# Performance work log

Hardware: AMD Instinct MI355X
Metric: run time of the kernel (lower is better)

The kernel has to match this reference:

```python
import jax, jax.numpy as jnp
import numpy as np

GROUP_SIZE = 128


def dequantize_int4(packed, scales, group_size=GROUP_SIZE, dtype=jnp.float16):
    # packed: [O, I//2] bytes; low nibble -> even cols, high nibble -> odd cols
    O = packed.shape[0]
    I = packed.shape[1] * 2
    low = (packed & 15).astype(jnp.int8) - 8
    high = ((packed >> 4) & 15).astype(jnp.int8) - 8
    unpacked = jnp.stack([low, high], axis=-1).reshape(O, I)  # interleave low/high
    G = I // group_size
    grouped = unpacked.reshape(O, G, group_size).astype(jnp.float32)
    deq = grouped * scales.astype(jnp.float32)[:, :, None]  # per-group scale
    return deq.reshape(O, I).astype(dtype)


def setup_inputs() -> dict:
    key = jax.random.key(0)
    k1, k2, k3 = jax.random.split(key, 3)
    B, S, IN, OUT = 4, 2048, 4096, 11008
    G = IN // GROUP_SIZE
    x = jax.random.normal(k1, (B, S, IN), dtype=jnp.float16)
    packed = jax.random.randint(k2, (OUT, IN // 2), 0, 256, dtype=jnp.int32)
    scales = (jax.random.uniform(k3, (OUT, G), dtype=jnp.float32) * 0.05 + 0.001).astype(jnp.float16)
    return {"x": x, "packed": packed, "scales": scales}


def reference(x, packed, scales):
    x = x.astype(jnp.float16)
    W = dequantize_int4(packed, scales)  # [OUT, IN] fp16
    # nn.functional.linear: x @ W^T
    return jnp.einsum('bsi,oi->bso', x, W)
```

## Files before the change

kernel.cpp:

```cpp
#include <hip/hip_runtime.h>

#define M_DIM 8192
#define N_DIM 11008
#define K_DIM 4096
#define GROUPS 32
#define WQROW 512
#define LDSK 72

typedef short s16x8 __attribute__((ext_vector_type(8)));
typedef _Float16 f16x8 __attribute__((ext_vector_type(8)));
typedef _Float16 h2 __attribute__((ext_vector_type(2)));
typedef float f32x4 __attribute__((ext_vector_type(4)));
typedef unsigned short u16;
typedef unsigned int u32;

union f32u { float f; unsigned u; };
union h16u { u16 u; _Float16 h; };

__device__ __forceinline__ u16 f2bf(float f) {
  f32u v; v.f = f;
  unsigned r = v.u + 0x7FFFu + ((v.u >> 16) & 1u);
  return (u16)(r >> 16);
}
__device__ __forceinline__ float bf2f(u16 b) {
  f32u v; v.u = ((unsigned)b) << 16; return v.f;
}
__device__ __forceinline__ float h2f(u16 b) {
  h16u v; v.u = b; return (float)v.h;
}

__global__ void probe_mode_kernel(const void* __restrict__ scales,
                                  int* __restrict__ mode_out) {
  __shared__ int cnt[3];
  int t = threadIdx.x;
  if (t < 3) cnt[t] = 0;
  __syncthreads();
  float f0 = ((const float*)scales)[t];
  u16  hu  = ((const u16*)scales)[t];
  float f1 = h2f(hu);
  float f2 = bf2f(hu);
  if (f0 > 0.0004f && f0 < 0.065f) atomicAdd(&cnt[0], 1);
  if (f1 > 0.0004f && f1 < 0.065f) atomicAdd(&cnt[1], 1);
  if (f2 > 0.0004f && f2 < 0.065f) atomicAdd(&cnt[2], 1);
  __syncthreads();
  if (t == 0) {
    int m;
    if      (cnt[1] >= 240) m = 1;
    else if (cnt[2] >= 240) m = 2;
    else                    m = 0;
    mode_out[0] = m;
  }
}

__global__ __launch_bounds__(256) void convert_x_nat_kernel(
    const float* __restrict__ xf, u16* __restrict__ xh,
    const int* __restrict__ modep) {
  if (modep && modep[0] != 0) return;
  const int total8 = M_DIM * (K_DIM / 8);
  int idx = blockIdx.x * 256 + threadIdx.x;
  const int stride = gridDim.x * 256;
  for (; idx < total8; idx += stride) {
    const float4* p = (const float4*)(xf + (size_t)idx * 8);
    float4 a = p[0], b = p[1];
    union { _Float16 h[8]; s16x8 v; } r;
    r.h[0] = (_Float16)a.x; r.h[1] = (_Float16)a.y;
    r.h[2] = (_Float16)a.z; r.h[3] = (_Float16)a.w;
    r.h[4] = (_Float16)b.x; r.h[5] = (_Float16)b.y;
    r.h[6] = (_Float16)b.z; r.h[7] = (_Float16)b.w;
    *(s16x8*)(xh + (size_t)idx * 8) = r.v;
  }
}

__global__ __launch_bounds__(256) void dequant_w_kernel(
    const int* __restrict__ packed, const float* __restrict__ scf,
    u16* __restrict__ wf, const int* __restrict__ modep) {
  if (modep && modep[0] != 0) return;
  const int total = N_DIM * (K_DIM / 8);
  int idx = blockIdx.x * 256 + threadIdx.x;
  const int stride = gridDim.x * 256;
  for (; idx < total; idx += stride) {
    const int col = idx >> 9;
    const int d   = idx & 511;
    const float s = scf[col * GROUPS + (d >> 4)];
    const int4 p  = ((const int4*)packed)[idx];
    const int vals[4] = {p.x, p.y, p.z, p.w};
    union { _Float16 h[8]; s16x8 v; } r;
    #pragma unroll
    for (int e = 0; e < 4; ++e) {
      int b = vals[e] & 255;
      r.h[2 * e]     = (_Float16)((float)((b & 15) - 8) * s);
      r.h[2 * e + 1] = (_Float16)((float)(((b >> 4) & 15) - 8) * s);
    }
    *(s16x8*)(wf + (size_t)idx * 8) = r.v;
  }
}

__global__ __launch_bounds__(512, 2) void q4gemm_big_kernel(
    const u16* __restrict__ xh,
    const u16* __restrict__ wf,
    float* __restrict__ out,
    const int* __restrict__ modep)
{
  if (modep && modep[0] != 0) return;

  __shared__ _Float16 AsA[2][256 * 64];
  __shared__ _Float16 AsB[2][256 * 64];

  const int tid  = threadIdx.x;
  const int lane = tid & 63;
  const int wv   = tid >> 6;
  const int wm   = (wv >> 2) * 128;
  const int wn   = (wv & 3) * 64;
  const int ln15 = lane & 15;
  const int lk   = lane >> 4;

  int bid = blockIdx.x;
  int f   = (bid & 7) * 172 + (bid >> 3);
  int bn  = f / 32;
  int bm  = f - bn * 32;
  const int m0 = bm * 256;
  const int n0 = bn * 256;

  const int srow  = lane >> 3;
  const int sperm = (lane & 7) ^ srow;
  const u16* abase[4];
  const u16* bbase[4];
  #pragma unroll
  for (int q = 0; q < 4; ++q) {
    int row = q * 64 + wv * 8 + srow;
    abase[q] = xh + (size_t)(m0 + row) * K_DIM + sperm * 8;
    bbase[q] = wf + (size_t)(n0 + row) * K_DIM + sperm * 8;
  }

#define STAGE_ALL(PB, T) do { \
    _Float16* da = &AsA[(PB)][0]; \
    _Float16* db = &AsB[(PB)][0]; \
    _Pragma("unroll") \
    for (int q = 0; q < 4; ++q) \
      __builtin_amdgcn_global_load_lds( \
          (const __attribute__((address_space(1))) void*)(abase[q] + (T) * 64), \
          (__attribute__((address_space(3))) void*)(da + q * 4096 + wv * 512), \
          16, 0, 0); \
    _Pragma("unroll") \
    for (int q = 0; q < 4; ++q) \
      __builtin_amdgcn_global_load_lds( \
          (const __attribute__((address_space(1))) void*)(bbase[q] + (T) * 64), \
          (__attribute__((address_space(3))) void*)(db + q * 4096 + wv * 512), \
          16, 0, 0); \
  } while (0)

#define TILE_BODY(CUR) do { \
    const _Float16* Ab = &AsA[(CUR)][0]; \
    const _Float16* Bb = &AsB[(CUR)][0]; \
    const int slotx = ln15 & 7; \
    const int slot0 = lk ^ slotx; \
    const int slot1 = (4 + lk) ^ slotx; \
    f16x8 bf0[4], bf1[4], afA[4], afB[4]; \
    _Pragma("unroll") \
    for (int j = 0; j < 4; ++j) \
      bf0[j] = *(const f16x8*)&Bb[(wn + j * 16 + ln15) * 64 + slot0 * 8]; \
    _Pragma("unroll") \
    for (int ii = 0; ii < 4; ++ii) \
      afA[ii] = *(const f16x8*)&Ab[(wm + ii * 16 + ln15) * 64 + slot0 * 8]; \
    __builtin_amdgcn_s_setprio(1); \
    _Pragma("unroll") \
    for (int ii = 0; ii < 4; ++ii) { \
      acc[ii][0] = __builtin_amdgcn_mfma_f32_16x16x32_f16(afA[ii], bf0[0], acc[ii][0], 0, 0, 0); \
      acc[ii][1] = __builtin_amdgcn_mfma_f32_16x16x32_f16(afA[ii], bf0[1], acc[ii][1], 0, 0, 0); \
      acc[ii][2] = __builtin_amdgcn_mfma_f32_16x16x32_f16(afA[ii], bf0[2], acc[ii][2], 0, 0, 0); \
      acc[ii][3] = __builtin_amdgcn_mfma_f32_16x16x32_f16(afA[ii], bf0[3], acc[ii][3], 0, 0, 0); \
    } \
    _Pragma("unroll") \
    for (int ii = 0; ii < 4; ++ii) \
      afB[ii] = *(const f16x8*)&Ab[(wm + (4 + ii) * 16 + ln15) * 64 + slot0 * 8]; \
    _Pragma("unroll") \
    for (int ii = 0; ii < 4; ++ii) { \
      acc[4 + ii][0] = __builtin_amdgcn_mfma_f32_16x16x32_f16(afB[ii], bf0[0], acc[4 + ii][0], 0, 0, 0); \
      acc[4 + ii][1] = __builtin_amdgcn_mfma_f32_16x16x32_f16(afB[ii], bf0[1], acc[4 + ii][1], 0, 0, 0); \
      acc[4 + ii][2] = __builtin_amdgcn_mfma_f32_16x16x32_f16(afB[ii], bf0[2], acc[4 + ii][2], 0, 0, 0); \
      acc[4 + ii][3] = __builtin_amdgcn_mfma_f32_16x16x32_f16(afB[ii], bf0[3], acc[4 + ii][3], 0, 0, 0); \
    } \
    _Pragma("unroll") \
    for (int j = 0; j < 4; ++j) \
      bf1[j] = *(const f16x8*)&Bb[(wn + j * 16 + ln15) * 64 + slot1 * 8]; \
    _Pragma("unroll") \
    for (int ii = 0; ii < 4; ++ii) \
      afA[ii] = *(const f16x8*)&Ab[(wm + ii * 16 + ln15) * 64 + slot1 * 8]; \
    _Pragma("unroll") \
    for (int ii = 0; ii < 4; ++ii) { \
      acc[ii][0] = __builtin_amdgcn_mfma_f32_16x16x32_f16(afA[ii], bf1[0], acc[ii][0], 0, 0, 0); \
      acc[ii][1] = __builtin_amdgcn_mfma_f32_16x16x32_f16(afA[ii], bf1[1], acc[ii][1], 0, 0, 0); \
      acc[ii][2] = __builtin_amdgcn_mfma_f32_16x16x32_f16(afA[ii], bf1[2], acc[ii][2], 0, 0, 0); \
      acc[ii][3] = __builtin_amdgcn_mfma_f32_16x16x32_f16(afA[ii], bf1[3], acc[ii][3], 0, 0, 0); \
    } \
    _Pragma("unroll") \
    for (int ii = 0; ii < 4; ++ii) \
      afB[ii] = *(const f16x8*)&Ab[(wm + (4 + ii) * 16 + ln15) * 64 + slot1 * 8]; \
    _Pragma("unroll") \
    for (int ii = 0; ii < 4; ++ii) { \
      acc[4 + ii][0] = __builtin_amdgcn_mfma_f32_16x16x32_f16(afB[ii], bf1[0], acc[4 + ii][0], 0, 0, 0); \
      acc[4 + ii][1] = __builtin_amdgcn_mfma_f32_16x16x32_f16(afB[ii], bf1[1], acc[4 + ii][1], 0, 0, 0); \
      acc[4 + ii][2] = __builtin_amdgcn_mfma_f32_16x16x32_f16(afB[ii], bf1[2], acc[4 + ii][2], 0, 0, 0); \
      acc[4 + ii][3] = __builtin_amdgcn_mfma_f32_16x16x32_f16(afB[ii], bf1[3], acc[4 + ii][3], 0, 0, 0); \
    } \
    __builtin_amdgcn_s_setprio(0); \
  } while (0)

  f32x4 acc[8][4];
  #pragma unroll
  for (int i = 0; i < 8; ++i)
    #pragma unroll
    for (int j = 0; j < 4; ++j)
      acc[i][j] = f32x4{0.f, 0.f, 0.f, 0.f};

  STAGE_ALL(0, 0);

  #pragma unroll 1
  for (int tp = 0; tp < 32; ++tp) {
    const int t0 = 2 * tp;

    asm volatile("s_waitcnt vmcnt(0)" ::: "memory");
    __builtin_amdgcn_s_barrier();
    STAGE_ALL(1, t0 + 1);
    TILE_BODY(0);

    asm volatile("s_waitcnt vmcnt(0)" ::: "memory");
    __builtin_amdgcn_s_barrier();
    if (t0 + 2 < 64) STAGE_ALL(0, t0 + 2);
    TILE_BODY(1);
  }

  #pragma unroll
  for (int i = 0; i < 8; ++i) {
    int r0 = m0 + wm + i * 16 + (lane >> 4) * 4;
    #pragma unroll
    for (int j = 0; j < 4; ++j) {
      int cc = n0 + wn + j * 16 + ln15;
      #pragma unroll
      for (int r = 0; r < 4; ++r)
        __builtin_nontemporal_store(acc[i][j][r], &out[(size_t)(r0 + r) * N_DIM + cc]);
    }
  }
#undef STAGE_ALL
#undef TILE_BODY
}

__global__ __launch_bounds__(256) void convert_x_perm_kernel(
    const float* __restrict__ xf, u16* __restrict__ xh,
    const int* __restrict__ modep) {
  if (modep && modep[0] != 0) return;
  const int total8 = M_DIM * (K_DIM / 8);
  int idx = blockIdx.x * 256 + threadIdx.x;
  const int stride = gridDim.x * 256;
  for (; idx < total8; idx += stride) {
    const float4* p = (const float4*)(xf + (size_t)idx * 8);
    float4 a = p[0], b = p[1];
    union { _Float16 h[8]; s16x8 v; } r;
    r.h[0] = (_Float16)a.x; r.h[1] = (_Float16)b.x;
    r.h[2] = (_Float16)a.y; r.h[3] = (_Float16)b.y;
    r.h[4] = (_Float16)a.z; r.h[5] = (_Float16)b.z;
    r.h[6] = (_Float16)a.w; r.h[7] = (_Float16)b.w;
    *(s16x8*)(xh + (size_t)idx * 8) = r.v;
  }
}

__global__ __launch_bounds__(256) void repack_w_kernel(
    const int* __restrict__ packed, u32* __restrict__ wq) {
  const int total = N_DIM * WQROW;
  int idx = blockIdx.x * 256 + threadIdx.x;
  const int stride = gridDim.x * 256;
  for (; idx < total; idx += stride) {
    const int4 p = ((const int4*)packed)[idx];
    wq[idx] = (u32)(p.x & 255) | ((u32)(p.y & 255) << 8) |
              ((u32)(p.z & 255) << 16) | ((u32)p.w << 24);
  }
}

__device__ __forceinline__ f16x8 dq8(u32 q, h2 s2) {
  const u32 M = 0x000F000Fu, G = 0x64006400u;
  const h2 bias = {(_Float16)(-1032.0f), (_Float16)(-1032.0f)};
  union { u32 u; h2 h; } a0, a1, a2, a3;
  a0.u = (q & M) | G;
  a1.u = ((q >> 4) & M) | G;
  a2.u = ((q >> 8) & M) | G;
  a3.u = ((q >> 12) & M) | G;
  a0.h = (a0.h + bias) * s2;
  a1.h = (a1.h + bias) * s2;
  a2.h = (a2.h + bias) * s2;
  a3.h = (a3.h + bias) * s2;
  union { u32 u[4]; f16x8 f; } r;
  r.u[0] = a0.u; r.u[1] = a1.u; r.u[2] = a2.u; r.u[3] = a3.u;
  return r.f;
}

__global__ __launch_bounds__(256, 2) void q4gemm_mid_kernel(
    const u16* __restrict__ xh, const u32* __restrict__ wq,
    const float* __restrict__ scf, float* __restrict__ out,
    const int* __restrict__ modep)
{
  if (modep && modep[0] != 0) return;

  __shared__ _Float16 As[3][128 * 64];

  const int tid  = threadIdx.x;
  const int lane = tid & 63;
  const int wv   = tid >> 6;
  const int wn   = wv * 64;
  const int ln15 = lane & 15;
  const int lk   = lane >> 4;

  int bid = blockIdx.x;
  int f   = (bid & 7) * 344 + (bid >> 3);
  int bn  = f / 64;
  int bm  = f - bn * 64;
  const int m0 = bm * 128;
  const int n0 = bn * 256;

  const u16* abase[4];
  #pragma unroll
  for (int q = 0; q < 4; ++q) {
    int row = q * 32 + wv * 8 + (lane >> 3);
    abase[q] = xh + (size_t)(m0 + row) * K_DIM + (((lane & 7) ^ (lane >> 3)) * 8);
  }

#define STAGE(PB, T) do { \
    _Float16* dst = &As[(PB)][0]; \
    _Pragma("unroll") \
    for (int q = 0; q < 4; ++q) \
      __builtin_amdgcn_global_load_lds( \
          (const __attribute__((address_space(1))) void*)(abase[q] + (T) * 64), \
          (__attribute__((address_space(3))) void*)(dst + q * 2048 + wv * 512), \
          16, 0, 0); \
  } while (0)

#define LOADB(RB, T) do { \
    _Pragma("unroll") \
    for (int j = 0; j < 4; ++j) { \
      RB[j]     = wq[pcol[j] + (T) * 8]; \
      RB[j + 4] = wq[pcol[j] + (T) * 8 + 4]; \
    } \
  } while (0)

#define COMPUTE(RB, PB) do { \
    const _Float16* asb = &As[(PB)][0]; \
    _Pragma("unroll") \
    for (int kkc = 0; kkc < 2; ++kkc) { \
      f16x8 bfr0 = dq8(RB[kkc * 4 + 0], s2[0]); \
      f16x8 bfr1 = dq8(RB[kkc * 4 + 1], s2[1]); \
      f16x8 bfr2 = dq8(RB[kkc * 4 + 2], s2[2]); \
      f16x8 bfr3 = dq8(RB[kkc * 4 + 3], s2[3]); \
      _Pragma("unroll") \
      for (int i = 0; i < 8; ++i) { \
        const int row  = i * 16 + ln15; \
        const int slot = (kkc * 4 + lk) ^ (ln15 & 7); \
        f16x8 af = *(const f16x8*)&asb[row * 64 + slot * 8]; \
        acc[i][0] = __builtin_amdgcn_mfma_f32_16x16x32_f16(af, bfr0, acc[i][0], 0, 0, 0); \
        acc[i][1] = __builtin_amdgcn_mfma_f32_16x16x32_f16(af, bfr1, acc[i][1], 0, 0, 0); \
        acc[i][2] = __builtin_amdgcn_mfma_f32_16x16x32_f16(af, bfr2, acc[i][2], 0, 0, 0); \
        acc[i][3] = __builtin_amdgcn_mfma_f32_16x16x32_f16(af, bfr3, acc[i][3], 0, 0, 0); \
      } \
    } \
  } while (0)

  int pcol[4], scol[4];
  #pragma unroll
  for (int j = 0; j < 4; ++j) {
    int col = n0 + wn + j * 16 + ln15;
    pcol[j] = col * WQROW + lk;
    scol[j] = col * GROUPS;
  }

  f32x4 acc[8][4];
  #pragma unroll
  for (int i = 0; i < 8; ++i)
    #pragma unroll
    for (int j = 0; j < 4; ++j)
      acc[i][j] = f32x4{0.f, 0.f, 0.f, 0.f};

  u32 rbE[8], rbO[8];
  float snextf[4];
  h2 s2[4];

  STAGE(0, 0);
  STAGE(1, 1);
  LOADB(rbE, 0);
  LOADB(rbO, 1);
  #pragma unroll
  for (int j = 0; j < 4; ++j) snextf[j] = scf[scol[j]];
  asm volatile("s_waitcnt vmcnt(0)" ::: "memory");

  int p0 = 0, p1 = 1, p2 = 2;

  for (int tp = 0; tp < 32; ++tp) {
    const int t0 = 2 * tp;
    const int t1 = t0 + 1;

    asm volatile("s_waitcnt vmcnt(12)" ::: "memory");
    __builtin_amdgcn_s_barrier();
    __builtin_amdgcn_sched_barrier(0);

    #pragma unroll
    for (int j = 0; j < 4; ++j) {
      _Float16 sh = (_Float16)snextf[j];
      s2[j] = h2{sh, sh};
    }
    if (t0 + 2 < 64) STAGE(p2, t0 + 2);

    __builtin_amdgcn_s_setprio(1);
    COMPUTE(rbE, p0);
    __builtin_amdgcn_s_setprio(0);

    if (t0 + 2 < 64) LOADB(rbE, t0 + 2);
    {
      const int gn = (tp + 1 > 31) ? 31 : (tp + 1);
      #pragma unroll
      for (int j = 0; j < 4; ++j) snextf[j] = scf[scol[j] + gn];
    }

    if (tp == 31) {
      asm volatile("s_waitcnt vmcnt(0)" ::: "memory");
    } else {
      asm volatile("s_waitcnt vmcnt(12)" ::: "memory");
    }
    __builtin_amdgcn_s_barrier();
    __builtin_amdgcn_sched_barrier(0);

    if (t1 + 2 < 64) STAGE(p0, t1 + 2);

    __builtin_amdgcn_s_setprio(1);
    COMPUTE(rbO, p1);
    __builtin_amdgcn_s_setprio(0);

    if (t1 + 2 < 64) LOADB(rbO, t1 + 2);

    int tmp = p2; p2 = p1; p1 = p0; p0 = tmp;
  }

  #pragma unroll
  for (int i = 0; i < 8; ++i) {
    int r0 = m0 + i * 16 + (lane >> 4) * 4;
    #pragma unroll
    for (int j = 0; j < 4; ++j) {
      int cc = n0 + wn + j * 16 + ln15;
      #pragma unroll
      for (int r = 0; r < 4; ++r)
        out[(size_t)(r0 + r) * N_DIM + cc] = acc[i][j][r];
    }
  }
#undef STAGE
#undef LOADB
#undef COMPUTE
}

__global__ __launch_bounds__(256) void q4gemm_slow_kernel(
    const void* __restrict__ xraw,
    const int*  __restrict__ packed,
    const void* __restrict__ scraw,
    float* __restrict__ out,
    const int* __restrict__ modep,
    int skip0)
{
  const int mode = modep ? modep[0] : 0;
  if (skip0 && mode == 0) return;

  __shared__ u16 Asl[128 * LDSK];
  __shared__ u16 Bsl[128 * LDSK];

  const int tid  = threadIdx.x;
  const int lane = tid & 63;
  const int wv   = tid >> 6;
  const int wm   = (wv >> 1) * 64;
  const int wn   = (wv & 1) * 64;
  const int n0   = blockIdx.x * 128;
  const int m0   = blockIdx.y * 128;

  f32x4 acc[4][4];
  #pragma unroll
  for (int i = 0; i < 4; ++i)
    #pragma unroll
    for (int j = 0; j < 4; ++j)
      acc[i][j] = f32x4{0.f, 0.f, 0.f, 0.f};

  const int lrow16 = lane & 15;
  const int lk8    = (lane >> 4) * 8;

  for (int k0 = 0; k0 < K_DIM; k0 += 64) {
    if (mode == 0) {
      const float* xf = (const float*)xraw;
      #pragma unroll
      for (int it = 0; it < 4; ++it) {
        int s = tid + it * 256;
        int row = s >> 3, c8 = (s & 7) * 8;
        const float4* p = (const float4*)(xf + (size_t)(m0 + row) * K_DIM + k0 + c8);
        float4 v0 = p[0], v1 = p[1];
        u16 tmp[8] = { f2bf(v0.x), f2bf(v0.y), f2bf(v0.z), f2bf(v0.w),
                       f2bf(v1.x), f2bf(v1.y), f2bf(v1.z), f2bf(v1.w) };
        *(s16x8*)&Asl[row * LDSK + c8] = *(const s16x8*)tmp;
      }
    } else if (mode == 1) {
      const u16* xhh = (const u16*)xraw;
      #pragma unroll
      for (int it = 0; it < 4; ++it) {
        int s = tid + it * 256;
        int row = s >> 3, c8 = (s & 7) * 8;
        s16x8 v = *(const s16x8*)(xhh + (size_t)(m0 + row) * K_DIM + k0 + c8);
        u16 tmp[8];
        #pragma unroll
        for (int j = 0; j < 8; ++j) tmp[j] = f2bf(h2f((u16)v[j]));
        *(s16x8*)&Asl[row * LDSK + c8] = *(const s16x8*)tmp;
      }
    } else {
      const u16* xhh = (const u16*)xraw;
      #pragma unroll
      for (int it = 0; it < 4; ++it) {
        int s = tid + it * 256;
        int row = s >> 3, c8 = (s & 7) * 8;
        s16x8 v = *(const s16x8*)(xhh + (size_t)(m0 + row) * K_DIM + k0 + c8);
        *(s16x8*)&Asl[row * LDSK + c8] = v;
      }
    }

    {
      int row  = tid >> 1;
      int half = tid & 1;
      int srw  = n0 + row;
      int g    = k0 >> 7;
      float scale;
      if      (mode == 0) scale = ((const float*)scraw)[(size_t)srw * GROUPS + g];
      else if (mode == 1) scale = h2f(((const u16*)scraw)[(size_t)srw * GROUPS + g]);
      else                scale = bf2f(((const u16*)scraw)[(size_t)srw * GROUPS + g]);

      const int4* pp = (const int4*)(packed + (size_t)srw * (K_DIM / 2) + (k0 >> 1) + half * 16);
      #pragma unroll
      for (int j = 0; j < 4; ++j) {
        int4 pv = pp[j];
        int vals[4] = {pv.x, pv.y, pv.z, pv.w};
        u16 w[8];
        #pragma unroll
        for (int e = 0; e < 4; ++e) {
          int b = vals[e] & 255;
          w[e * 2]     = f2bf(scale * (float)((b & 15) - 8));
          w[e * 2 + 1] = f2bf(scale * (float)(((b >> 4) & 15) - 8));
        }
        int i0 = half * 16 + j * 4;
        *(s16x8*)&Bsl[row * LDSK + i0 * 2] = *(const s16x8*)w;
      }
    }
    __syncthreads();

    #pragma unroll
    for (int kk = 0; kk < 64; kk += 32) {
      s16x8 af[4], bfr[4];
      int klane = kk + lk8;
      #pragma unroll
      for (int i = 0; i < 4; ++i)
        af[i] = *(const s16x8*)&Asl[(wm + i * 16 + lrow16) * LDSK + klane];
      #pragma unroll
      for (int i = 0; i < 4; ++i)
        bfr[i] = *(const s16x8*)&Bsl[(wn + i * 16 + lrow16) * LDSK + klane];
      #pragma unroll
      for (int i = 0; i < 4; ++i)
        #pragma unroll
        for (int j = 0; j < 4; ++j)
          acc[i][j] = __builtin_amdgcn_mfma_f32_16x16x32_bf16(af[i], bfr[j], acc[i][j], 0, 0, 0);
    }
    __syncthreads();
  }

  #pragma unroll
  for (int i = 0; i < 4; ++i) {
    int rbase = m0 + wm + i * 16 + ((lane >> 4) * 4);
    #pragma unroll
    for (int j = 0; j < 4; ++j) {
      int c = n0 + wn + j * 16 + (lane & 15);
      #pragma unroll
      for (int r = 0; r < 4; ++r)
        out[(size_t)(rbase + r) * N_DIM + c] = acc[i][j][r];
    }
  }
}

extern "C" void kernel_launch(void* const* d_in, const int* in_sizes, int n_in,
                              void* d_out, int out_size, void* d_ws, size_t ws_size,
                              hipStream_t stream) {
  const void* x      = d_in[0];
  const int*  packed = (const int*)d_in[1];
  const void* scales = d_in[2];
  float* out = (float*)d_out;

  const size_t XB = (size_t)M_DIM * K_DIM * 2;
  const size_t WF = (size_t)N_DIM * K_DIM * 2;
  const size_t WQ = (size_t)N_DIM * WQROW * 4;
  const size_t NEED_BIG = 256 + XB + WF;
  const size_t NEED_MID = 256 + XB + WQ;

  int* mode_flag = nullptr;
  if (ws_size >= 4) {
    mode_flag = (int*)d_ws;
    probe_mode_kernel<<<dim3(1), dim3(256), 0, stream>>>(scales, mode_flag);
  }

  int fast = 0;
  if (mode_flag && ws_size >= NEED_BIG) fast = 2;
  else if (mode_flag && ws_size >= NEED_MID) fast = 1;

  if (fast == 2) {
    u16* xh = (u16*)((char*)d_ws + 256);
    u16* wf = (u16*)((char*)d_ws + 256 + XB);
    convert_x_nat_kernel<<<dim3(2048), dim3(256), 0, stream>>>(
        (const float*)x, xh, mode_flag);
    dequant_w_kernel<<<dim3(2048), dim3(256), 0, stream>>>(
        packed, (const float*)scales, wf, mode_flag);
    q4gemm_big_kernel<<<dim3(1376), dim3(512), 0, stream>>>(
        xh, wf, out, mode_flag);
  } else if (fast == 1) {
    u16* xh = (u16*)((char*)d_ws + 256);
    u32* wq = (u32*)((char*)d_ws + 256 + XB);
    convert_x_perm_kernel<<<dim3(2048), dim3(256), 0, stream>>>(
        (const float*)x, xh, mode_flag);
    repack_w_kernel<<<dim3(2048), dim3(256), 0, stream>>>(packed, wq);
    q4gemm_mid_kernel<<<dim3(2752), dim3(256), 0, stream>>>(
        xh, wq, (const float*)scales, out, mode_flag);
  }

  q4gemm_slow_kernel<<<dim3(N_DIM / 128, M_DIM / 128), dim3(256), 0, stream>>>(
      x, packed, scales, out, mode_flag, fast);
}
```

Measured before the change: 829.2 us.

## Load B fragments directly from global memory instead of staging through LDS

Removes the LDS double buffer for the weight tile and has each wave load its B fragments straight from global memory into registers at the start of each K tile. This halves LDS usage and LDS write/read traffic per tile, which could allow more occupancy and fewer LDS bank cycles. In exchange, the four waves sharing the same N columns now each fetch B redundantly from global/L2, and those global loads are issued synchronously inside the compute body with no prefetch, so their latency sits on the critical path.

Result: slower. 1.192 ms (+43.7%).

```diff
diff --git a/kernel.cpp b/kernel.cpp
--- a/kernel.cpp
+++ b/kernel.cpp
@@ -104,7 +104,6 @@
   if (modep && modep[0] != 0) return;
 
   __shared__ _Float16 AsA[2][256 * 64];
-  __shared__ _Float16 AsB[2][256 * 64];
 
   const int tid  = threadIdx.x;
   const int lane = tid & 63;
@@ -124,41 +123,40 @@
   const int srow  = lane >> 3;
   const int sperm = (lane & 7) ^ srow;
   const u16* abase[4];
-  const u16* bbase[4];
   #pragma unroll
   for (int q = 0; q < 4; ++q) {
     int row = q * 64 + wv * 8 + srow;
     abase[q] = xh + (size_t)(m0 + row) * K_DIM + sperm * 8;
-    bbase[q] = wf + (size_t)(n0 + row) * K_DIM + sperm * 8;
-  }
-
-#define STAGE_ALL(PB, T) do { \
+  }
+
+  const u16* pB[4];
+  #pragma unroll
+  for (int j = 0; j < 4; ++j) {
+    int col = n0 + wn + j * 16 + ln15;
+    pB[j] = wf + (size_t)col * K_DIM + lk * 8;
+  }
+
+#define STAGE_A(PB, T) do { \
     _Float16* da = &AsA[(PB)][0]; \
-    _Float16* db = &AsB[(PB)][0]; \
     _Pragma("unroll") \
     for (int q = 0; q < 4; ++q) \
       __builtin_amdgcn_global_load_lds( \
           (const __attribute__((address_space(1))) void*)(abase[q] + (T) * 64), \
           (__attribute__((address_space(3))) void*)(da + q * 4096 + wv * 512), \
           16, 0, 0); \
-    _Pragma("unroll") \
-    for (int q = 0; q < 4; ++q) \
-      __builtin_amdgcn_global_load_lds( \
-          (const __attribute__((address_space(1))) void*)(bbase[q] + (T) * 64), \
-          (__attribute__((address_space(3))) void*)(db + q * 4096 + wv * 512), \
-          16, 0, 0); \
   } while (0)
 
-#define TILE_BODY(CUR) do { \
+#define TILE_BODY(CUR, T) do { \
     const _Float16* Ab = &AsA[(CUR)][0]; \
-    const _Float16* Bb = &AsB[(CUR)][0]; \
     const int slotx = ln15 & 7; \
     const int slot0 = lk ^ slotx; \
     const int slot1 = (4 + lk) ^ slotx; \
     f16x8 bf0[4], bf1[4], afA[4], afB[4]; \
     _Pragma("unroll") \
-    for (int j = 0; j < 4; ++j) \
-      bf0[j] = *(const f16x8*)&Bb[(wn + j * 16 + ln15) * 64 + slot0 * 8]; \
+    for (int j = 0; j < 4; ++j) { \
+      bf0[j] = *(const f16x8*)(pB[j] + (T) * 64); \
+      bf1[j] = *(const f16x8*)(pB[j] + (T) * 64 + 32); \
+    } \
     _Pragma("unroll") \
     for (int ii = 0; ii < 4; ++ii) \
       afA[ii] = *(const f16x8*)&Ab[(wm + ii * 16 + ln15) * 64 + slot0 * 8]; \
@@ -180,9 +178,6 @@
       acc[4 + ii][2] = __builtin_amdgcn_mfma_f32_16x16x32_f16(afB[ii], bf0[2], acc[4 + ii][2], 0, 0, 0); \
       acc[4 + ii][3] = __builtin_amdgcn_mfma_f32_16x16x32_f16(afB[ii], bf0[3], acc[4 + ii][3], 0, 0, 0); \
     } \
-    _Pragma("unroll") \
-    for (int j = 0; j < 4; ++j) \
-      bf1[j] = *(const f16x8*)&Bb[(wn + j * 16 + ln15) * 64 + slot1 * 8]; \
     _Pragma("unroll") \
     for (int ii = 0; ii < 4; ++ii) \
       afA[ii] = *(const f16x8*)&Ab[(wm + ii * 16 + ln15) * 64 + slot1 * 8]; \
@@ -213,7 +208,7 @@
     for (int j = 0; j < 4; ++j)
       acc[i][j] = f32x4{0.f, 0.f, 0.f, 0.f};
 
-  STAGE_ALL(0, 0);
+  STAGE_A(0, 0);
 
   #pragma unroll 1
   for (int tp = 0; tp < 32; ++tp) {
@@ -221,13 +216,13 @@
 
     asm volatile("s_waitcnt vmcnt(0)" ::: "memory");
     __builtin_amdgcn_s_barrier();
-    STAGE_ALL(1, t0 + 1);
-    TILE_BODY(0);
+    STAGE_A(1, t0 + 1);
+    TILE_BODY(0, t0);
 
     asm volatile("s_waitcnt vmcnt(0)" ::: "memory");
     __builtin_amdgcn_s_barrier();
-    if (t0 + 2 < 64) STAGE_ALL(0, t0 + 2);
-    TILE_BODY(1);
+    if (t0 + 2 < 64) STAGE_A(0, t0 + 2);
+    TILE_BODY(1, t0 + 1);
   }
 
   #pragma unroll
@@ -241,7 +236,7 @@
         __builtin_nontemporal_store(acc[i][j][r], &out[(size_t)(r0 + r) * N_DIM + cc]);
     }
   }
-#undef STAGE_ALL
+#undef STAGE_A
 #undef TILE_BODY
 }
 
```
